# Kernel tuning notes

Measured on AMD Instinct MI355X. Metric: run time of the kernel, lower is better.

## Reference

```python
import jax, jax.numpy as jnp
import numpy as np

L_LAYERS = 2
EPS = 1e-6  # flax LayerNorm default epsilon


def _binop_reset(qi, qj):
    # S5 resettable associative scan element: (A, Bu, reset_flag)
    Ai, bi, ci = qi
    Aj, bj, cj = qj
    A = (Aj * Ai) * (1 - cj) + Aj * cj
    b = (Aj * bi + bj) * (1 - cj) + bj * cj
    c = ci * (1 - cj) + cj
    return A, b, c


def _layernorm(x, scale, bias):
    mu = jnp.mean(x, axis=-1, keepdims=True)
    var = jnp.var(x, axis=-1, keepdims=True)
    return (x - mu) * jax.lax.rsqrt(var + EPS) * scale + bias


def _s5_layer(x, resets, h0, lam_re, lam_im, B2, C2, Dv, log_step, nsc, nbi, gw, gb):
    # x: (B,T,H) float32; resets: (B,T) float32; h0: (B,1,P) complex64
    Bsz, T, H = x.shape
    P = lam_re.shape[0]
    skip = x
    xn = _layernorm(x, nsc, nbi)
    # ZOH discretization
    Lam = lam_re + 1j * lam_im                       # (P,)
    step = jnp.exp(log_step[:, 0])                   # (P,)
    Lam_bar = jnp.exp(Lam * step)                    # (P,)
    B_t = B2[..., 0] + 1j * B2[..., 1]               # (P,H)
    B_bar = ((Lam_bar - 1.0) / Lam)[:, None] * B_t   # (P,H)
    C_t = C2[..., 0] + 1j * C2[..., 1]               # (H,P)
    Bu = jnp.einsum('ph,bth->btp', B_bar, xn.astype(B_bar.dtype))  # (B,T,P) complex
    # prepend carry / identity elements, run reset-aware parallel scan over time
    ones = jnp.ones((Bsz, 1, P), dtype=Lam_bar.dtype)
    A_el = jnp.concatenate([ones, jnp.broadcast_to(Lam_bar, (Bsz, T, P))], axis=1)
    b_el = jnp.concatenate([h0, Bu], axis=1)
    c_el = jnp.concatenate([jnp.zeros((Bsz, 1, 1), x.dtype), resets[..., None]], axis=1)
    _, xs, _ = jax.lax.associative_scan(_binop_reset, (A_el, b_el, c_el), axis=1)
    xs = xs[:, 1:]                                   # (B,T,P) states
    h_new = xs[:, -1:, :]                            # (B,1,P) new carry
    ys = 2.0 * jnp.einsum('hp,btp->bth', C_t, xs).real  # conj_sym output
    y = ys + Dv * xn                                 # skip-through D
    # half_glu1 activation
    y = jax.nn.gelu(y)
    y = y * jax.nn.sigmoid(y @ gw + gb)
    return h_new, skip + y


def setup_inputs() -> dict:
    key = jax.random.key(0)
    B, T, OBS, H, P, L = 128, 1024, 512, 64, 128, L_LAYERS
    ks = jax.random.split(key, 10)
    obs = jax.random.normal(ks[0], (B, T, OBS), jnp.float32)
    dones = (jax.random.uniform(ks[1], (B, T)) < 0.02).astype(jnp.int32)
    hidden = jnp.zeros((L, B, 1, P, 2), jnp.float32)
    dense_w = jax.random.normal(ks[2], (OBS, H), jnp.float32) * np.float32(1.0 / np.sqrt(OBS))
    dense_b = jnp.zeros((H,), jnp.float32)
    Lambda_re = -(0.5 + jax.random.uniform(ks[3], (L, P), jnp.float32))  # stable (negative) real parts
    Lambda_im = np.float32(np.pi) * jax.random.normal(ks[4], (L, P), jnp.float32)
    Bp = jax.random.normal(ks[5], (L, P, H, 2), jnp.float32) * np.float32(1.0 / np.sqrt(H))
    Cp = jax.random.normal(ks[6], (L, H, P, 2), jnp.float32) * np.float32(1.0 / np.sqrt(P))
    D = jax.random.normal(ks[7], (L, H), jnp.float32)
    log_step = jax.random.uniform(ks[8], (L, P, 1), jnp.float32,
                                  minval=np.float32(np.log(0.001)), maxval=np.float32(np.log(0.1)))
    norm_scale = jnp.ones((L, H), jnp.float32)
    norm_bias = jnp.zeros((L, H), jnp.float32)
    glu_w = jax.random.normal(ks[9], (L, H, H), jnp.float32) * np.float32(1.0 / np.sqrt(H))
    glu_b = jnp.zeros((L, H), jnp.float32)
    return {"obs": obs, "dones": dones, "hidden": hidden, "dense_w": dense_w, "dense_b": dense_b,
            "Lambda_re": Lambda_re, "Lambda_im": Lambda_im, "Bp": Bp, "Cp": Cp, "D": D,
            "log_step": log_step, "norm_scale": norm_scale, "norm_bias": norm_bias,
            "glu_w": glu_w, "glu_b": glu_b}


def reference(obs, dones, hidden, dense_w, dense_b, Lambda_re, Lambda_im, Bp, Cp, D,
              log_step, norm_scale, norm_bias, glu_w, glu_b):
    x = obs @ dense_w + dense_b                      # dense_0 embedding (B,T,H)
    resets = dones.astype(x.dtype)
    h = hidden[..., 0] + 1j * hidden[..., 1]         # (L,B,1,P) complex carries
    new_h = []
    for l in range(L_LAYERS):
        hl, x = _s5_layer(x, resets, h[l], Lambda_re[l], Lambda_im[l], Bp[l], Cp[l], D[l],
                          log_step[l], norm_scale[l], norm_bias[l], glu_w[l], glu_b[l])
        new_h.append(hl)
    h_out = jnp.stack(new_h, axis=0)                 # (L,B,1,P) complex
    h_out = jnp.stack([h_out.real, h_out.imag], axis=-1)
    return h_out, x
```

## Files before the change

kernel.cpp:

```cpp
#include <hip/hip_runtime.h>

#define NB 128
#define NT 1024
#define NOBS 512
#define NH 64
#define NP 128
#define NM (NB*NT)
#define NN2 256
#define NCH 16
#define CHL 64

typedef short bf16x8 __attribute__((ext_vector_type(8)));
typedef float f32x4 __attribute__((ext_vector_type(4)));

#define CONST_OFF ((size_t)91226112)
#define CONST_STRIDE ((size_t)131072)
#define WTB_OFF   ((size_t)92274688)

__device__ __forceinline__ unsigned short f2b(float f) {
  unsigned int u = __float_as_uint(f);
  u = u + 0x7fffu + ((u >> 16) & 1u);
  return (unsigned short)(u >> 16);
}
__device__ __forceinline__ float b2f(unsigned short s) {
  return __uint_as_float(((unsigned int)s) << 16);
}

__global__ __launch_bounds__(256) void k_setup(const float* Lre, const float* Lim,
    const float* Bp, const float* Cp, const float* lstep, const float* gw,
    const float* dw, unsigned char* wsb) {
  int l = blockIdx.y;
  int idx = blockIdx.x * 256 + threadIdx.x;
  unsigned char* cb = wsb + CONST_OFF + (size_t)l * CONST_STRIDE;
  float2* lambar = (float2*)cb;
  unsigned short* Bglob = (unsigned short*)(cb + 1024);
  unsigned short* Cglob = (unsigned short*)(cb + 33792);
  unsigned short* gwT   = (unsigned short*)(cb + 66560);
  {
    int n = idx >> 6, h = idx & 63, p = n >> 1, c = n & 1;
    float step = expf(lstep[l * NP + p]);
    float re = Lre[l * NP + p], im = Lim[l * NP + p];
    float er = expf(re * step), ang = im * step;
    float lbr = er * cosf(ang), lbi = er * sinf(ang);
    if (h == 0 && c == 0) lambar[p] = make_float2(lbr, lbi);
    float den = re * re + im * im;
    float nr = lbr - 1.f, ni = lbi;
    float dr = (nr * re + ni * im) / den;
    float di = (ni * re - nr * im) / den;
    size_t bb = ((size_t)(l * NP + p) * NH + h) * 2;
    float b0 = Bp[bb + 0], b1 = Bp[bb + 1];
    float vr = dr * b0 - di * b1;
    float vi = dr * b1 + di * b0;
    Bglob[n * 64 + h] = f2b(c ? vi : vr);
  }
  {
    int h = idx >> 8, n = idx & 255, p = n >> 1;
    size_t base = ((size_t)(l * NH + h) * NP + p) * 2;
    float val = (n & 1) ? (-2.f * Cp[base + 1]) : (2.f * Cp[base + 0]);
    Cglob[h * 256 + n] = f2b(val);
  }
  if (idx < 4096) {
    int n = idx >> 6, k = idx & 63;
    gwT[n * 64 + k] = f2b(gw[(size_t)(l * NH + k) * NH + n]);
  }
  {
    int idx2 = l * 16384 + idx;
    int h = idx2 >> 9, k = idx2 & 511;
    ((unsigned short*)(wsb + WTB_OFF))[h * 512 + k] = f2b(dw[(size_t)k * NH + h]);
  }
}

__global__ __launch_bounds__(256) void k_dense(const float* __restrict__ obs,
    const unsigned short* __restrict__ wTb, const float* __restrict__ bias,
    float* __restrict__ xout) {
  __shared__ __align__(16) unsigned short As[128][72];
  __shared__ __align__(16) unsigned short Bs[64][72];
  int tid = threadIdx.x, lane = tid & 63, wv = tid >> 6;
  int row0 = blockIdx.x * 128;
  f32x4 acc[2][4] = {};
  float bcol[4];
#pragma unroll
  for (int ct = 0; ct < 4; ++ct) bcol[ct] = bias[ct * 16 + (lane & 15)];
  float4 ra[8];
  uint4 rb[2];
#pragma unroll
  for (int i = 0; i < 8; ++i) {
    int id = tid + i * 256;
    ra[i] = *(const float4*)(obs + (size_t)(row0 + (id >> 4)) * NOBS + (id & 15) * 4);
  }
#pragma unroll
  for (int i = 0; i < 2; ++i) {
    int id = tid + i * 256;
    rb[i] = *(const uint4*)(wTb + (id >> 3) * 512 + (id & 7) * 8);
  }
  for (int kt = 0; kt < 8; ++kt) {
#pragma unroll
    for (int i = 0; i < 8; ++i) {
      int id = tid + i * 256;
      ushort4 o; o.x = f2b(ra[i].x); o.y = f2b(ra[i].y); o.z = f2b(ra[i].z); o.w = f2b(ra[i].w);
      *(ushort4*)&As[id >> 4][(id & 15) * 4] = o;
    }
#pragma unroll
    for (int i = 0; i < 2; ++i) {
      int id = tid + i * 256;
      *(uint4*)&Bs[id >> 3][(id & 7) * 8] = rb[i];
    }
    __syncthreads();
    if (kt < 7) {
      int k0 = (kt + 1) * 64;
#pragma unroll
      for (int i = 0; i < 8; ++i) {
        int id = tid + i * 256;
        ra[i] = *(const float4*)(obs + (size_t)(row0 + (id >> 4)) * NOBS + k0 + (id & 15) * 4);
      }
#pragma unroll
      for (int i = 0; i < 2; ++i) {
        int id = tid + i * 256;
        rb[i] = *(const uint4*)(wTb + (id >> 3) * 512 + k0 + (id & 7) * 8);
      }
    }
#pragma unroll
    for (int kc = 0; kc < 2; ++kc) {
      bf16x8 a0 = *(const bf16x8*)&As[wv * 32 + (lane & 15)][kc * 32 + (lane >> 4) * 8];
      bf16x8 a1 = *(const bf16x8*)&As[wv * 32 + 16 + (lane & 15)][kc * 32 + (lane >> 4) * 8];
#pragma unroll
      for (int ct = 0; ct < 4; ++ct) {
        bf16x8 bb = *(const bf16x8*)&Bs[ct * 16 + (lane & 15)][kc * 32 + (lane >> 4) * 8];
        acc[0][ct] = __builtin_amdgcn_mfma_f32_16x16x32_bf16(a0, bb, acc[0][ct], 0, 0, 0);
        acc[1][ct] = __builtin_amdgcn_mfma_f32_16x16x32_bf16(a1, bb, acc[1][ct], 0, 0, 0);
      }
    }
    __syncthreads();
  }
  float* Os = (float*)&As[0][0];
#pragma unroll
  for (int pass = 0; pass < 2; ++pass) {
    if ((wv >> 1) == pass) {
#pragma unroll
      for (int rt = 0; rt < 2; ++rt)
#pragma unroll
        for (int ct = 0; ct < 4; ++ct)
#pragma unroll
          for (int e = 0; e < 4; ++e) {
            int rl = (wv & 1) * 32 + rt * 16 + (lane >> 4) * 4 + e;
            int col = ct * 16 + (lane & 15);
            Os[rl * 68 + col] = acc[rt][ct][e] + bcol[ct];
          }
    }
    __syncthreads();
    {
      int r = tid >> 2, seg = tid & 3;
#pragma unroll
      for (int i = 0; i < 4; ++i)
        *(float4*)(xout + (size_t)(row0 + pass * 64 + r) * NH + seg * 16 + i * 4) =
            *(const float4*)&Os[r * 68 + seg * 16 + i * 4];
    }
    __syncthreads();
  }
}

__global__ __launch_bounds__(512, 2) void k_2layers(float* __restrict__ x,
    const int* __restrict__ dones, const unsigned char* __restrict__ cb0,
    const float* __restrict__ hidden, float* __restrict__ hout,
    const float* __restrict__ nsc0, const float* __restrict__ nbi0,
    const float* __restrict__ Dv0, const float* __restrict__ gb0) {
  __shared__ __align__(16) unsigned short Bs[256][72];
  __shared__ __align__(16) unsigned short Cs[64][264];
  __shared__ __align__(16) unsigned short BuS[2][64][264];
  __shared__ __align__(16) unsigned short xnS[64][72];
  __shared__ __align__(16) unsigned short Ys[64][72];
  __shared__ int dS[1024];
  __shared__ float murs[4][64][2];
  int tid = threadIdx.x, lane = tid & 63, wv = tid >> 6;
  int b = blockIdx.x;

  dS[tid] = dones[b * NT + tid];
  dS[tid + 512] = dones[b * NT + 512 + tid];

#pragma unroll 1
  for (int l = 0; l < 2; ++l) {
    const unsigned char* cb = cb0 + (size_t)l * CONST_STRIDE;
    const float* nsc = nsc0 + l * NH;
    const float* nbi = nbi0 + l * NH;
    const float* Dv  = Dv0 + l * NH;
    const float* gb  = gb0 + l * NH;
    const unsigned short* Bglob = (const unsigned short*)(cb + 1024);
    const unsigned short* Cglob = (const unsigned short*)(cb + 33792);
    const unsigned short* gwT = (const unsigned short*)(cb + 66560);

    {
      int r = tid >> 1, h0 = (tid & 1) * 32;
#pragma unroll
      for (int i = 0; i < 4; ++i)
        *(uint4*)&Bs[r][h0 + i * 8] = *(const uint4*)(Bglob + r * 64 + h0 + i * 8);
    }
    {
      int r = tid >> 3, s0 = (tid & 7) * 32;
#pragma unroll
      for (int i = 0; i < 4; ++i)
        *(uint4*)&Cs[r][s0 + i * 8] = *(const uint4*)(Cglob + r * 256 + s0 + i * 8);
    }

    float4 pre0, pre1, pre2, pre3;
    float nscr[16], nbir[16];
    float lamr = 0.f, lami = 0.f, hr = 0.f, hi = 0.f;
    float Dr[4], nscc[4], nbic[4], gbr[4];
    if (tid < 256) {
      int q = tid & 3;
#pragma unroll
      for (int j = 0; j < 16; ++j) { nscr[j] = nsc[q * 16 + j]; nbir[j] = nbi[q * 16 + j]; }
      int r = tid >> 2;
      const float* xr = x + ((size_t)b * NT + r) * NH + q * 16;
      pre0 = *(const float4*)(xr);     pre1 = *(const float4*)(xr + 4);
      pre2 = *(const float4*)(xr + 8); pre3 = *(const float4*)(xr + 12);
    } else {
#pragma unroll
      for (int ct = 0; ct < 4; ++ct) {
        int col = ct * 16 + (lane & 15);
        Dr[ct] = Dv[col]; nscc[ct] = nsc[col]; nbic[ct] = nbi[col]; gbr[ct] = gb[col];
      }
      if (tid < 384) {
        int p = tid - 256;
        float2 lm = ((const float2*)cb)[p];
        lamr = lm.x; lami = lm.y;
        size_t hoff = (((size_t)l * NB + b) * NP + p) * 2;
        hr = hidden[hoff]; hi = hidden[hoff + 1];
      }
    }
    __syncthreads();

#pragma unroll 1
    for (int i = 0; i < NCH + 2; ++i) {
      float yreg[4][4], xres[4][4];
      if (tid < 256) {
        if (i < NCH) {
          float vv[16];
          *(float4*)&vv[0] = pre0;  *(float4*)&vv[4] = pre1;
          *(float4*)&vv[8] = pre2;  *(float4*)&vv[12] = pre3;
          int r = tid >> 2, q = tid & 3;
          if (i < NCH - 1) {
            const float* xr = x + ((size_t)b * NT + (i + 1) * CHL + r) * NH + q * 16;
            pre0 = *(const float4*)(xr);     pre1 = *(const float4*)(xr + 4);
            pre2 = *(const float4*)(xr + 8); pre3 = *(const float4*)(xr + 12);
          }
          float s = 0.f, s2 = 0.f;
#pragma unroll
          for (int j = 0; j < 16; ++j) { s += vv[j]; s2 += vv[j] * vv[j]; }
          s += __shfl_xor(s, 1); s2 += __shfl_xor(s2, 1);
          s += __shfl_xor(s, 2); s2 += __shfl_xor(s2, 2);
          float mu = s * 0.015625f;
          float var = s2 * 0.015625f - mu * mu;
          float rs = rsqrtf(var + 1e-6f);
          if (q == 0) { murs[i & 3][r][0] = mu; murs[i & 3][r][1] = rs; }
#pragma unroll
          for (int j = 0; j < 16; ++j)
            xnS[r][q * 16 + j] = f2b((vv[j] - mu) * rs * nscr[j] + nbir[j]);
        }
      } else if (i >= 2) {
        int j = i - 2, wv2 = wv - 4;
#pragma unroll
        for (int ct = 0; ct < 4; ++ct)
#pragma unroll
          for (int e = 0; e < 4; ++e) {
            int rl = wv2 * 16 + (lane >> 4) * 4 + e;
            xres[ct][e] = x[((size_t)b * NT + j * CHL + rl) * NH + ct * 16 + (lane & 15)];
          }
        f32x4 acc[4] = {};
        const unsigned short (*Bu)[264] = BuS[j & 1];
#pragma unroll
        for (int kc = 0; kc < 8; ++kc) {
          bf16x8 a = *(const bf16x8*)&Bu[wv2 * 16 + (lane & 15)][kc * 32 + (lane >> 4) * 8];
#pragma unroll
          for (int ct = 0; ct < 4; ++ct) {
            bf16x8 bbf = *(const bf16x8*)&Cs[ct * 16 + (lane & 15)][kc * 32 + (lane >> 4) * 8];
            acc[ct] = __builtin_amdgcn_mfma_f32_16x16x32_bf16(a, bbf, acc[ct], 0, 0, 0);
          }
        }
#pragma unroll
        for (int ct = 0; ct < 4; ++ct)
#pragma unroll
          for (int e = 0; e < 4; ++e) {
            int rl = wv2 * 16 + (lane >> 4) * 4 + e;
            float mu = murs[j & 3][rl][0], rs = murs[j & 3][rl][1];
            float xnv = (xres[ct][e] - mu) * rs * nscc[ct] + nbic[ct];
            float yv = acc[ct][e] + Dr[ct] * xnv;
            float t3 = 0.7978845608f * (yv + 0.044715f * yv * yv * yv);
            float u = __expf(2.f * t3);
            yv = 0.5f * yv * (2.f - 2.f / (u + 1.f));
            yreg[ct][e] = yv;
            Ys[rl][ct * 16 + (lane & 15)] = f2b(yv);
          }
      }
      __syncthreads();
      if (tid >= 256 && i >= 2) {
        int j = i - 2, wv2 = wv - 4;
        f32x4 gacc[4] = {};
#pragma unroll
        for (int kc = 0; kc < 2; ++kc) {
          bf16x8 a = *(const bf16x8*)&Ys[wv2 * 16 + (lane & 15)][kc * 32 + (lane >> 4) * 8];
#pragma unroll
          for (int ct = 0; ct < 4; ++ct) {
            bf16x8 bbf = *(const bf16x8*)(gwT + (ct * 16 + (lane & 15)) * 64 + kc * 32 + (lane >> 4) * 8);
            gacc[ct] = __builtin_amdgcn_mfma_f32_16x16x32_bf16(a, bbf, gacc[ct], 0, 0, 0);
          }
        }
#pragma unroll
        for (int ct = 0; ct < 4; ++ct)
#pragma unroll
          for (int e = 0; e < 4; ++e) {
            int rl = wv2 * 16 + (lane >> 4) * 4 + e;
            float g = gacc[ct][e] + gbr[ct];
            float sg = 1.f / (1.f + __expf(-g));
            x[((size_t)b * NT + j * CHL + rl) * NH + ct * 16 + (lane & 15)] =
                xres[ct][e] + yreg[ct][e] * sg;
          }
      }
      __syncthreads();
      if (tid < 256) {
        if (i < NCH) {
          f32x4 acc[16] = {};
#pragma unroll
          for (int kc = 0; kc < 2; ++kc) {
            bf16x8 a = *(const bf16x8*)&xnS[wv * 16 + (lane & 15)][kc * 32 + (lane >> 4) * 8];
#pragma unroll
            for (int ct = 0; ct < 16; ++ct) {
              bf16x8 bbf = *(const bf16x8*)&Bs[ct * 16 + (lane & 15)][kc * 32 + (lane >> 4) * 8];
              acc[ct] = __builtin_amdgcn_mfma_f32_16x16x32_bf16(a, bbf, acc[ct], 0, 0, 0);
            }
          }
          unsigned short (*Bu)[264] = BuS[i & 1];
#pragma unroll
          for (int ct = 0; ct < 16; ++ct)
#pragma unroll
            for (int e = 0; e < 4; ++e)
              Bu[wv * 16 + (lane >> 4) * 4 + e][ct * 16 + (lane & 15)] = f2b(acc[ct][e]);
        }
      } else if (tid < 384 && i >= 1 && i <= NCH) {
        int ch = i - 1, p = tid - 256;
        unsigned short (*Bu)[264] = BuS[ch & 1];
#pragma unroll 4
        for (int t = 0; t < CHL; ++t) {
          unsigned int u = *(const unsigned int*)&Bu[t][2 * p];
          float bur = b2f((unsigned short)(u & 0xffffu));
          float bui = b2f((unsigned short)(u >> 16));
          if (dS[ch * CHL + t]) { hr = bur; hi = bui; }
          else {
            float nr = lamr * hr - lami * hi + bur;
            hi = lamr * hi + lami * hr + bui; hr = nr;
          }
          *(unsigned int*)&Bu[t][2 * p] = (unsigned int)f2b(hr) | ((unsigned int)f2b(hi) << 16);
        }
        if (i == NCH) {
          size_t hoff = (((size_t)l * NB + b) * NP + p) * 2;
          hout[hoff] = hr; hout[hoff + 1] = hi;
        }
      }
      __syncthreads();
    }
  }
}

extern "C" void kernel_launch(void* const* d_in, const int* in_sizes, int n_in,
                              void* d_out, int out_size, void* d_ws, size_t ws_size,
                              hipStream_t stream) {
  const float* obs    = (const float*)d_in[0];
  const int*   dones  = (const int*)d_in[1];
  const float* hidden = (const float*)d_in[2];
  const float* dw     = (const float*)d_in[3];
  const float* db     = (const float*)d_in[4];
  const float* Lre    = (const float*)d_in[5];
  const float* Lim    = (const float*)d_in[6];
  const float* Bp     = (const float*)d_in[7];
  const float* Cp     = (const float*)d_in[8];
  const float* Dv     = (const float*)d_in[9];
  const float* lstep  = (const float*)d_in[10];
  const float* nsc    = (const float*)d_in[11];
  const float* nbi    = (const float*)d_in[12];
  const float* gw     = (const float*)d_in[13];
  const float* gb     = (const float*)d_in[14];

  float* hout = (float*)d_out;
  float* x = hout + (size_t)2 * NB * NP * 2;

  unsigned char* wsb = (unsigned char*)d_ws;
  unsigned short* wTb = (unsigned short*)(wsb + WTB_OFF);

  k_setup<<<dim3(64, 2), 256, 0, stream>>>(Lre, Lim, Bp, Cp, lstep, gw, dw, wsb);
  k_dense<<<NM / 128, 256, 0, stream>>>(obs, wTb, db, x);
  k_2layers<<<NB, 512, 0, stream>>>(x, dones, wsb + CONST_OFF, hidden, hout,
                                    nsc, nbi, Dv, gb);
}
```

Before: 320.8 us.

## Run the two S5 layers as concurrent blocks linked by per-chunk flags

```diff
diff --git a/kernel.cpp b/kernel.cpp
--- a/kernel.cpp
+++ b/kernel.cpp
@@ -1,4 +1,5 @@
 #include <hip/hip_runtime.h>
+#include <hip/hip_bf16.h>
 
 #define NB 128
 #define NT 1024
@@ -13,6 +14,7 @@
 typedef short bf16x8 __attribute__((ext_vector_type(8)));
 typedef float f32x4 __attribute__((ext_vector_type(4)));
 
+#define FLAG_OFF  ((size_t)83886080)
 #define CONST_OFF ((size_t)91226112)
 #define CONST_STRIDE ((size_t)131072)
 #define WTB_OFF   ((size_t)92274688)
@@ -24,6 +26,9 @@
 }
 __device__ __forceinline__ float b2f(unsigned short s) {
   return __uint_as_float(((unsigned int)s) << 16);
+}
+__device__ __forceinline__ unsigned int pk2(float lo, float hi) {
+  return (unsigned int)f2b(lo) | ((unsigned int)f2b(hi) << 16);
 }
 
 __global__ __launch_bounds__(256) void k_setup(const float* Lre, const float* Lim,
@@ -36,6 +41,7 @@
   unsigned short* Bglob = (unsigned short*)(cb + 1024);
   unsigned short* Cglob = (unsigned short*)(cb + 33792);
   unsigned short* gwT   = (unsigned short*)(cb + 66560);
+  if (l == 0 && idx < NB * NCH) ((int*)(wsb + FLAG_OFF))[idx] = 0;
   {
     int n = idx >> 6, h = idx & 63, p = n >> 1, c = n & 1;
     float step = expf(lstep[l * NP + p]);
@@ -159,11 +165,12 @@
   }
 }
 
-__global__ __launch_bounds__(512, 2) void k_2layers(float* __restrict__ x,
+__global__ __launch_bounds__(512, 1) void k_layer(float* __restrict__ x,
     const int* __restrict__ dones, const unsigned char* __restrict__ cb0,
     const float* __restrict__ hidden, float* __restrict__ hout,
     const float* __restrict__ nsc0, const float* __restrict__ nbi0,
-    const float* __restrict__ Dv0, const float* __restrict__ gb0) {
+    const float* __restrict__ Dv0, const float* __restrict__ gb0,
+    int* __restrict__ flagv) {
   __shared__ __align__(16) unsigned short Bs[256][72];
   __shared__ __align__(16) unsigned short Cs[64][264];
   __shared__ __align__(16) unsigned short BuS[2][64][264];
@@ -173,190 +180,204 @@
   __shared__ float murs[4][64][2];
   int tid = threadIdx.x, lane = tid & 63, wv = tid >> 6;
   int b = blockIdx.x;
-
+  int l = blockIdx.y;
+  const unsigned char* cb = cb0 + (size_t)l * CONST_STRIDE;
+  const float* nsc = nsc0 + l * NH;
+  const float* nbi = nbi0 + l * NH;
+  const float* Dv  = Dv0 + l * NH;
+  const float* gb  = gb0 + l * NH;
+  const unsigned short* Bglob = (const unsigned short*)(cb + 1024);
+  const unsigned short* Cglob = (const unsigned short*)(cb + 33792);
+  const unsigned short* gwT = (const unsigned short*)(cb + 66560);
+  int* flg = flagv + b * NCH;
+
+  {
+    int r = tid >> 1, h0 = (tid & 1) * 32;
+#pragma unroll
+    for (int i = 0; i < 4; ++i)
+      *(uint4*)&Bs[r][h0 + i * 8] = *(const uint4*)(Bglob + r * 64 + h0 + i * 8);
+  }
+  {
+    int r = tid >> 3, s0 = (tid & 7) * 32;
+#pragma unroll
+    for (int i = 0; i < 4; ++i)
+      *(uint4*)&Cs[r][s0 + i * 8] = *(const uint4*)(Cglob + r * 256 + s0 + i * 8);
+  }
   dS[tid] = dones[b * NT + tid];
   dS[tid + 512] = dones[b * NT + 512 + tid];
 
+  if (l == 1) {
+    while (__hip_atomic_load(&flg[0], __ATOMIC_RELAXED, __HIP_MEMORY_SCOPE_AGENT) == 0)
+      __builtin_amdgcn_s_sleep(8);
+    (void)__hip_atomic_load(&flg[0], __ATOMIC_ACQUIRE, __HIP_MEMORY_SCOPE_AGENT);
+  }
+
+  float4 pre0, pre1, pre2, pre3;
+  float nscr[16], nbir[16];
+  float lamr = 0.f, lami = 0.f, hr = 0.f, hi = 0.f;
+  float Dr[4], nscc[4], nbic[4], gbr[4];
+  if (tid < 256) {
+    int q = tid & 3;
+#pragma unroll
+    for (int j = 0; j < 16; ++j) { nscr[j] = nsc[q * 16 + j]; nbir[j] = nbi[q * 16 + j]; }
+    int r = tid >> 2;
+    const float* xr = x + ((size_t)b * NT + r) * NH + q * 16;
+    pre0 = *(const float4*)(xr);     pre1 = *(const float4*)(xr + 4);
+    pre2 = *(const float4*)(xr + 8); pre3 = *(const float4*)(xr + 12);
+  } else {
+#pragma unroll
+    for (int ct = 0; ct < 4; ++ct) {
+      int col = ct * 16 + (lane & 15);
+      Dr[ct] = Dv[col]; nscc[ct] = nsc[col]; nbic[ct] = nbi[col]; gbr[ct] = gb[col];
+    }
+    if (tid < 384) {
+      int p = tid - 256;
+      float2 lm = ((const float2*)cb)[p];
+      lamr = lm.x; lami = lm.y;
+      size_t hoff = (((size_t)l * NB + b) * NP + p) * 2;
+      hr = hidden[hoff]; hi = hidden[hoff + 1];
+    }
+  }
+  __syncthreads();
+
 #pragma unroll 1
-  for (int l = 0; l < 2; ++l) {
-    const unsigned char* cb = cb0 + (size_t)l * CONST_STRIDE;
-    const float* nsc = nsc0 + l * NH;
-    const float* nbi = nbi0 + l * NH;
-    const float* Dv  = Dv0 + l * NH;
-    const float* gb  = gb0 + l * NH;
-    const unsigned short* Bglob = (const unsigned short*)(cb + 1024);
-    const unsigned short* Cglob = (const unsigned short*)(cb + 33792);
-    const unsigned short* gwT = (const unsigned short*)(cb + 66560);
-
-    {
-      int r = tid >> 1, h0 = (tid & 1) * 32;
-#pragma unroll
-      for (int i = 0; i < 4; ++i)
-        *(uint4*)&Bs[r][h0 + i * 8] = *(const uint4*)(Bglob + r * 64 + h0 + i * 8);
-    }
-    {
-      int r = tid >> 3, s0 = (tid & 7) * 32;
-#pragma unroll
-      for (int i = 0; i < 4; ++i)
-        *(uint4*)&Cs[r][s0 + i * 8] = *(const uint4*)(Cglob + r * 256 + s0 + i * 8);
-    }
-
-    float4 pre0, pre1, pre2, pre3;
-    float nscr[16], nbir[16];
-    float lamr = 0.f, lami = 0.f, hr = 0.f, hi = 0.f;
-    float Dr[4], nscc[4], nbic[4], gbr[4];
+  for (int i = 0; i < NCH + 2; ++i) {
+    if (l == 1 && i < NCH - 1) {
+      while (__hip_atomic_load(&flg[i + 1], __ATOMIC_RELAXED, __HIP_MEMORY_SCOPE_AGENT) == 0)
+        __builtin_amdgcn_s_sleep(8);
+      (void)__hip_atomic_load(&flg[i + 1], __ATOMIC_ACQUIRE, __HIP_MEMORY_SCOPE_AGENT);
+    }
+    float yreg[4][4], xres[4][4];
     if (tid < 256) {
-      int q = tid & 3;
-#pragma unroll
-      for (int j = 0; j < 16; ++j) { nscr[j] = nsc[q * 16 + j]; nbir[j] = nbi[q * 16 + j]; }
-      int r = tid >> 2;
-      const float* xr = x + ((size_t)b * NT + r) * NH + q * 16;
-      pre0 = *(const float4*)(xr);     pre1 = *(const float4*)(xr + 4);
-      pre2 = *(const float4*)(xr + 8); pre3 = *(const float4*)(xr + 12);
-    } else {
-#pragma unroll
-      for (int ct = 0; ct < 4; ++ct) {
-        int col = ct * 16 + (lane & 15);
-        Dr[ct] = Dv[col]; nscc[ct] = nsc[col]; nbic[ct] = nbi[col]; gbr[ct] = gb[col];
-      }
-      if (tid < 384) {
-        int p = tid - 256;
-        float2 lm = ((const float2*)cb)[p];
-        lamr = lm.x; lami = lm.y;
+      if (i < NCH) {
+        float vv[16];
+        *(float4*)&vv[0] = pre0;  *(float4*)&vv[4] = pre1;
+        *(float4*)&vv[8] = pre2;  *(float4*)&vv[12] = pre3;
+        int r = tid >> 2, q = tid & 3;
+        if (i < NCH - 1) {
+          const float* xr = x + ((size_t)b * NT + (i + 1) * CHL + r) * NH + q * 16;
+          pre0 = *(const float4*)(xr);     pre1 = *(const float4*)(xr + 4);
+          pre2 = *(const float4*)(xr + 8); pre3 = *(const float4*)(xr + 12);
+        }
+        float s = 0.f, s2 = 0.f;
+#pragma unroll
+        for (int j = 0; j < 16; ++j) { s += vv[j]; s2 += vv[j] * vv[j]; }
+        s += __shfl_xor(s, 1); s2 += __shfl_xor(s2, 1);
+        s += __shfl_xor(s, 2); s2 += __shfl_xor(s2, 2);
+        float mu = s * 0.015625f;
+        float var = s2 * 0.015625f - mu * mu;
+        float rs = rsqrtf(var + 1e-6f);
+        if (q == 0) { murs[i & 3][r][0] = mu; murs[i & 3][r][1] = rs; }
+#pragma unroll
+        for (int k = 0; k < 8; ++k) {
+          float a0 = (vv[2 * k] - mu) * rs * nscr[2 * k] + nbir[2 * k];
+          float a1 = (vv[2 * k + 1] - mu) * rs * nscr[2 * k + 1] + nbir[2 * k + 1];
+          *(unsigned int*)&xnS[r][q * 16 + 2 * k] = pk2(a0, a1);
+        }
+      }
+    } else if (i >= 2) {
+      int j = i - 2, wv2 = wv - 4;
+#pragma unroll
+      for (int ct = 0; ct < 4; ++ct)
+#pragma unroll
+        for (int e = 0; e < 4; ++e) {
+          int rl = wv2 * 16 + (lane >> 4) * 4 + e;
+          xres[ct][e] = x[((size_t)b * NT + j * CHL + rl) * NH + ct * 16 + (lane & 15)];
+        }
+      f32x4 acc[4] = {};
+      const unsigned short (*Bu)[264] = BuS[j & 1];
+#pragma unroll
+      for (int kc = 0; kc < 8; ++kc) {
+        bf16x8 a = *(const bf16x8*)&Bu[wv2 * 16 + (lane & 15)][kc * 32 + (lane >> 4) * 8];
+#pragma unroll
+        for (int ct = 0; ct < 4; ++ct) {
+          bf16x8 bbf = *(const bf16x8*)&Cs[ct * 16 + (lane & 15)][kc * 32 + (lane >> 4) * 8];
+          acc[ct] = __builtin_amdgcn_mfma_f32_16x16x32_bf16(a, bbf, acc[ct], 0, 0, 0);
+        }
+      }
+#pragma unroll
+      for (int ct = 0; ct < 4; ++ct)
+#pragma unroll
+        for (int e = 0; e < 4; ++e) {
+          int rl = wv2 * 16 + (lane >> 4) * 4 + e;
+          float mu = murs[j & 3][rl][0], rs = murs[j & 3][rl][1];
+          float xnv = (xres[ct][e] - mu) * rs * nscc[ct] + nbic[ct];
+          float yv = acc[ct][e] + Dr[ct] * xnv;
+          float t3 = 0.7978845608f * (yv + 0.044715f * yv * yv * yv);
+          float u = __expf(2.f * t3);
+          yv = 0.5f * yv * (2.f - 2.f / (u + 1.f));
+          yreg[ct][e] = yv;
+          Ys[rl][ct * 16 + (lane & 15)] = f2b(yv);
+        }
+    }
+    __syncthreads();
+    if (tid >= 256 && i >= 2) {
+      int j = i - 2, wv2 = wv - 4;
+      f32x4 gacc[4] = {};
+#pragma unroll
+      for (int kc = 0; kc < 2; ++kc) {
+        bf16x8 a = *(const bf16x8*)&Ys[wv2 * 16 + (lane & 15)][kc * 32 + (lane >> 4) * 8];
+#pragma unroll
+        for (int ct = 0; ct < 4; ++ct) {
+          bf16x8 bbf = *(const bf16x8*)(gwT + (ct * 16 + (lane & 15)) * 64 + kc * 32 + (lane >> 4) * 8);
+          gacc[ct] = __builtin_amdgcn_mfma_f32_16x16x32_bf16(a, bbf, gacc[ct], 0, 0, 0);
+        }
+      }
+#pragma unroll
+      for (int ct = 0; ct < 4; ++ct)
+#pragma unroll
+        for (int e = 0; e < 4; ++e) {
+          int rl = wv2 * 16 + (lane >> 4) * 4 + e;
+          float g = gacc[ct][e] + gbr[ct];
+          float sg = 1.f / (1.f + __expf(-g));
+          x[((size_t)b * NT + j * CHL + rl) * NH + ct * 16 + (lane & 15)] =
+              xres[ct][e] + yreg[ct][e] * sg;
+        }
+    }
+    __syncthreads();
+    if (l == 0 && i >= 2 && tid == 511)
+      __hip_atomic_store(&flg[i - 2], 1, __ATOMIC_RELEASE, __HIP_MEMORY_SCOPE_AGENT);
+    if (tid < 256) {
+      if (i < NCH) {
+        f32x4 acc[16] = {};
+#pragma unroll
+        for (int kc = 0; kc < 2; ++kc) {
+          bf16x8 a = *(const bf16x8*)&xnS[wv * 16 + (lane & 15)][kc * 32 + (lane >> 4) * 8];
+#pragma unroll
+          for (int ct = 0; ct < 16; ++ct) {
+            bf16x8 bbf = *(const bf16x8*)&Bs[ct * 16 + (lane & 15)][kc * 32 + (lane >> 4) * 8];
+            acc[ct] = __builtin_amdgcn_mfma_f32_16x16x32_bf16(bbf, a, acc[ct], 0, 0, 0);
+          }
+        }
+        unsigned short (*Bu)[264] = BuS[i & 1];
+        int t = wv * 16 + (lane & 15), cb4 = (lane >> 4) * 4;
+#pragma unroll
+        for (int ct = 0; ct < 16; ++ct) {
+          *(unsigned int*)&Bu[t][ct * 16 + cb4]     = pk2(acc[ct][0], acc[ct][1]);
+          *(unsigned int*)&Bu[t][ct * 16 + cb4 + 2] = pk2(acc[ct][2], acc[ct][3]);
+        }
+      }
+    } else if (tid < 384 && i >= 1 && i <= NCH) {
+      int ch = i - 1, p = tid - 256;
+      unsigned short (*Bu)[264] = BuS[ch & 1];
+#pragma unroll 4
+      for (int t = 0; t < CHL; ++t) {
+        unsigned int u = *(const unsigned int*)&Bu[t][2 * p];
+        float bur = b2f((unsigned short)(u & 0xffffu));
+        float bui = b2f((unsigned short)(u >> 16));
+        if (dS[ch * CHL + t]) { hr = bur; hi = bui; }
+        else {
+          float nr = lamr * hr - lami * hi + bur;
+          hi = lamr * hi + lami * hr + bui; hr = nr;
+        }
+        *(unsigned int*)&Bu[t][2 * p] = pk2(hr, hi);
+      }
+      if (i == NCH) {
         size_t hoff = (((size_t)l * NB + b) * NP + p) * 2;
-        hr = hidden[hoff]; hi = hidden[hoff + 1];
-      }
-    }
-    __syncthreads();
-
-#pragma unroll 1
-    for (int i = 0; i < NCH + 2; ++i) {
-      float yreg[4][4], xres[4][4];
-      if (tid < 256) {
-        if (i < NCH) {
-          float vv[16];
-          *(float4*)&vv[0] = pre0;  *(float4*)&vv[4] = pre1;
-          *(float4*)&vv[8] = pre2;  *(float4*)&vv[12] = pre3;
-          int r = tid >> 2, q = tid & 3;
-          if (i < NCH - 1) {
-            const float* xr = x + ((size_t)b * NT + (i + 1) * CHL + r) * NH + q * 16;
-            pre0 = *(const float4*)(xr);     pre1 = *(const float4*)(xr + 4);
-            pre2 = *(const float4*)(xr + 8); pre3 = *(const float4*)(xr + 12);
-          }
-          float s = 0.f, s2 = 0.f;
-#pragma unroll
-          for (int j = 0; j < 16; ++j) { s += vv[j]; s2 += vv[j] * vv[j]; }
-          s += __shfl_xor(s, 1); s2 += __shfl_xor(s2, 1);
-          s += __shfl_xor(s, 2); s2 += __shfl_xor(s2, 2);
-          float mu = s * 0.015625f;
-          float var = s2 * 0.015625f - mu * mu;
-          float rs = rsqrtf(var + 1e-6f);
-          if (q == 0) { murs[i & 3][r][0] = mu; murs[i & 3][r][1] = rs; }
-#pragma unroll
-          for (int j = 0; j < 16; ++j)
-            xnS[r][q * 16 + j] = f2b((vv[j] - mu) * rs * nscr[j] + nbir[j]);
-        }
-      } else if (i >= 2) {
-        int j = i - 2, wv2 = wv - 4;
-#pragma unroll
-        for (int ct = 0; ct < 4; ++ct)
-#pragma unroll
-          for (int e = 0; e < 4; ++e) {
-            int rl = wv2 * 16 + (lane >> 4) * 4 + e;
-            xres[ct][e] = x[((size_t)b * NT + j * CHL + rl) * NH + ct * 16 + (lane & 15)];
-          }
-        f32x4 acc[4] = {};
-        const unsigned short (*Bu)[264] = BuS[j & 1];
-#pragma unroll
-        for (int kc = 0; kc < 8; ++kc) {
-          bf16x8 a = *(const bf16x8*)&Bu[wv2 * 16 + (lane & 15)][kc * 32 + (lane >> 4) * 8];
-#pragma unroll
-          for (int ct = 0; ct < 4; ++ct) {
-            bf16x8 bbf = *(const bf16x8*)&Cs[ct * 16 + (lane & 15)][kc * 32 + (lane >> 4) * 8];
-            acc[ct] = __builtin_amdgcn_mfma_f32_16x16x32_bf16(a, bbf, acc[ct], 0, 0, 0);
-          }
-        }
-#pragma unroll
-        for (int ct = 0; ct < 4; ++ct)
-#pragma unroll
-          for (int e = 0; e < 4; ++e) {
-            int rl = wv2 * 16 + (lane >> 4) * 4 + e;
-            float mu = murs[j & 3][rl][0], rs = murs[j & 3][rl][1];
-            float xnv = (xres[ct][e] - mu) * rs * nscc[ct] + nbic[ct];
-            float yv = acc[ct][e] + Dr[ct] * xnv;
-            float t3 = 0.7978845608f * (yv + 0.044715f * yv * yv * yv);
-            float u = __expf(2.f * t3);
-            yv = 0.5f * yv * (2.f - 2.f / (u + 1.f));
-            yreg[ct][e] = yv;
-            Ys[rl][ct * 16 + (lane & 15)] = f2b(yv);
-          }
-      }
-      __syncthreads();
-      if (tid >= 256 && i >= 2) {
-        int j = i - 2, wv2 = wv - 4;
-        f32x4 gacc[4] = {};
-#pragma unroll
-        for (int kc = 0; kc < 2; ++kc) {
-          bf16x8 a = *(const bf16x8*)&Ys[wv2 * 16 + (lane & 15)][kc * 32 + (lane >> 4) * 8];
-#pragma unroll
-          for (int ct = 0; ct < 4; ++ct) {
-            bf16x8 bbf = *(const bf16x8*)(gwT + (ct * 16 + (lane & 15)) * 64 + kc * 32 + (lane >> 4) * 8);
-            gacc[ct] = __builtin_amdgcn_mfma_f32_16x16x32_bf16(a, bbf, gacc[ct], 0, 0, 0);
-          }
-        }
-#pragma unroll
-        for (int ct = 0; ct < 4; ++ct)
-#pragma unroll
-          for (int e = 0; e < 4; ++e) {
-            int rl = wv2 * 16 + (lane >> 4) * 4 + e;
-            float g = gacc[ct][e] + gbr[ct];
-            float sg = 1.f / (1.f + __expf(-g));
-            x[((size_t)b * NT + j * CHL + rl) * NH + ct * 16 + (lane & 15)] =
-                xres[ct][e] + yreg[ct][e] * sg;
-          }
-      }
-      __syncthreads();
-      if (tid < 256) {
-        if (i < NCH) {
-          f32x4 acc[16] = {};
-#pragma unroll
-          for (int kc = 0; kc < 2; ++kc) {
-            bf16x8 a = *(const bf16x8*)&xnS[wv * 16 + (lane & 15)][kc * 32 + (lane >> 4) * 8];
-#pragma unroll
-            for (int ct = 0; ct < 16; ++ct) {
-              bf16x8 bbf = *(const bf16x8*)&Bs[ct * 16 + (lane & 15)][kc * 32 + (lane >> 4) * 8];
-              acc[ct] = __builtin_amdgcn_mfma_f32_16x16x32_bf16(a, bbf, acc[ct], 0, 0, 0);
-            }
-          }
-          unsigned short (*Bu)[264] = BuS[i & 1];
-#pragma unroll
-          for (int ct = 0; ct < 16; ++ct)
-#pragma unroll
-            for (int e = 0; e < 4; ++e)
-              Bu[wv * 16 + (lane >> 4) * 4 + e][ct * 16 + (lane & 15)] = f2b(acc[ct][e]);
-        }
-      } else if (tid < 384 && i >= 1 && i <= NCH) {
-        int ch = i - 1, p = tid - 256;
-        unsigned short (*Bu)[264] = BuS[ch & 1];
-#pragma unroll 4
-        for (int t = 0; t < CHL; ++t) {
-          unsigned int u = *(const unsigned int*)&Bu[t][2 * p];
-          float bur = b2f((unsigned short)(u & 0xffffu));
-          float bui = b2f((unsigned short)(u >> 16));
-          if (dS[ch * CHL + t]) { hr = bur; hi = bui; }
-          else {
-            float nr = lamr * hr - lami * hi + bur;
-            hi = lamr * hi + lami * hr + bui; hr = nr;
-          }
-          *(unsigned int*)&Bu[t][2 * p] = (unsigned int)f2b(hr) | ((unsigned int)f2b(hi) << 16);
-        }
-        if (i == NCH) {
-          size_t hoff = (((size_t)l * NB + b) * NP + p) * 2;
-          hout[hoff] = hr; hout[hoff + 1] = hi;
-        }
-      }
-      __syncthreads();
-    }
+        hout[hoff] = hr; hout[hoff + 1] = hi;
+      }
+    }
+    __syncthreads();
   }
 }
 
@@ -384,9 +405,10 @@
 
   unsigned char* wsb = (unsigned char*)d_ws;
   unsigned short* wTb = (unsigned short*)(wsb + WTB_OFF);
+  int* flagv = (int*)(wsb + FLAG_OFF);
 
   k_setup<<<dim3(64, 2), 256, 0, stream>>>(Lre, Lim, Bp, Cp, lstep, gw, dw, wsb);
   k_dense<<<NM / 128, 256, 0, stream>>>(obs, wTb, db, x);
-  k_2layers<<<NB, 512, 0, stream>>>(x, dones, wsb + CONST_OFF, hidden, hout,
-                                    nsc, nbi, Dv, gb);
-}
+  k_layer<<<dim3(NB, 2), 512, 0, stream>>>(x, dones, wsb + CONST_OFF, hidden, hout,
+                                           nsc, nbi, Dv, gb, flagv);
+}
```

Result: slower. 332.4 us (+3.6%).

## Fully unroll chunk scan with bitmask resets, register-cache GLU weights, pack bf16 stores

Applied to the files above, without the earlier changes.

```diff
diff --git a/kernel.cpp b/kernel.cpp
--- a/kernel.cpp
+++ b/kernel.cpp
@@ -24,6 +24,9 @@
 }
 __device__ __forceinline__ float b2f(unsigned short s) {
   return __uint_as_float(((unsigned int)s) << 16);
+}
+__device__ __forceinline__ unsigned int pk2(float lo, float hi) {
+  return (unsigned int)f2b(lo) | ((unsigned int)f2b(hi) << 16);
 }
 
 __global__ __launch_bounds__(256) void k_setup(const float* Lre, const float* Lim,
@@ -159,7 +162,7 @@
   }
 }
 
-__global__ __launch_bounds__(512, 2) void k_2layers(float* __restrict__ x,
+__global__ __launch_bounds__(512, 1) void k_2layers(float* __restrict__ x,
     const int* __restrict__ dones, const unsigned char* __restrict__ cb0,
     const float* __restrict__ hidden, float* __restrict__ hout,
     const float* __restrict__ nsc0, const float* __restrict__ nbi0,
@@ -169,13 +172,21 @@
   __shared__ __align__(16) unsigned short BuS[2][64][264];
   __shared__ __align__(16) unsigned short xnS[64][72];
   __shared__ __align__(16) unsigned short Ys[64][72];
-  __shared__ int dS[1024];
   __shared__ float murs[4][64][2];
+  __shared__ unsigned int dmask[32];
   int tid = threadIdx.x, lane = tid & 63, wv = tid >> 6;
   int b = blockIdx.x;
 
-  dS[tid] = dones[b * NT + tid];
-  dS[tid + 512] = dones[b * NT + 512 + tid];
+  {
+    unsigned long long m0 = __ballot(dones[b * NT + tid] != 0);
+    unsigned long long m1 = __ballot(dones[b * NT + 512 + tid] != 0);
+    if (lane == 0) {
+      dmask[wv * 2]          = (unsigned int)m0;
+      dmask[wv * 2 + 1]      = (unsigned int)(m0 >> 32);
+      dmask[16 + wv * 2]     = (unsigned int)m1;
+      dmask[16 + wv * 2 + 1] = (unsigned int)(m1 >> 32);
+    }
+  }
 
 #pragma unroll 1
   for (int l = 0; l < 2; ++l) {
@@ -205,6 +216,7 @@
     float nscr[16], nbir[16];
     float lamr = 0.f, lami = 0.f, hr = 0.f, hi = 0.f;
     float Dr[4], nscc[4], nbic[4], gbr[4];
+    bf16x8 gfr[2][4];
     if (tid < 256) {
       int q = tid & 3;
 #pragma unroll
@@ -219,6 +231,11 @@
         int col = ct * 16 + (lane & 15);
         Dr[ct] = Dv[col]; nscc[ct] = nsc[col]; nbic[ct] = nbi[col]; gbr[ct] = gb[col];
       }
+#pragma unroll
+      for (int kc = 0; kc < 2; ++kc)
+#pragma unroll
+        for (int ct = 0; ct < 4; ++ct)
+          gfr[kc][ct] = *(const bf16x8*)(gwT + (ct * 16 + (lane & 15)) * 64 + kc * 32 + (lane >> 4) * 8);
       if (tid < 384) {
         int p = tid - 256;
         float2 lm = ((const float2*)cb)[p];
@@ -253,8 +270,11 @@
           float rs = rsqrtf(var + 1e-6f);
           if (q == 0) { murs[i & 3][r][0] = mu; murs[i & 3][r][1] = rs; }
 #pragma unroll
-          for (int j = 0; j < 16; ++j)
-            xnS[r][q * 16 + j] = f2b((vv[j] - mu) * rs * nscr[j] + nbir[j]);
+          for (int k = 0; k < 8; ++k) {
+            float a0 = (vv[2 * k] - mu) * rs * nscr[2 * k] + nbir[2 * k];
+            float a1 = (vv[2 * k + 1] - mu) * rs * nscr[2 * k + 1] + nbir[2 * k + 1];
+            *(unsigned int*)&xnS[r][q * 16 + 2 * k] = pk2(a0, a1);
+          }
         }
       } else if (i >= 2) {
         int j = i - 2, wv2 = wv - 4;
@@ -299,10 +319,8 @@
         for (int kc = 0; kc < 2; ++kc) {
           bf16x8 a = *(const bf16x8*)&Ys[wv2 * 16 + (lane & 15)][kc * 32 + (lane >> 4) * 8];
 #pragma unroll
-          for (int ct = 0; ct < 4; ++ct) {
-            bf16x8 bbf = *(const bf16x8*)(gwT + (ct * 16 + (lane & 15)) * 64 + kc * 32 + (lane >> 4) * 8);
-            gacc[ct] = __builtin_amdgcn_mfma_f32_16x16x32_bf16(a, bbf, gacc[ct], 0, 0, 0);
-          }
+          for (int ct = 0; ct < 4; ++ct)
+            gacc[ct] = __builtin_amdgcn_mfma_f32_16x16x32_bf16(a, gfr[kc][ct], gacc[ct], 0, 0, 0);
         }
 #pragma unroll
         for (int ct = 0; ct < 4; ++ct)
@@ -325,32 +343,38 @@
 #pragma unroll
             for (int ct = 0; ct < 16; ++ct) {
               bf16x8 bbf = *(const bf16x8*)&Bs[ct * 16 + (lane & 15)][kc * 32 + (lane >> 4) * 8];
-              acc[ct] = __builtin_amdgcn_mfma_f32_16x16x32_bf16(a, bbf, acc[ct], 0, 0, 0);
+              acc[ct] = __builtin_amdgcn_mfma_f32_16x16x32_bf16(bbf, a, acc[ct], 0, 0, 0);
             }
           }
           unsigned short (*Bu)[264] = BuS[i & 1];
-#pragma unroll
-          for (int ct = 0; ct < 16; ++ct)
-#pragma unroll
-            for (int e = 0; e < 4; ++e)
-              Bu[wv * 16 + (lane >> 4) * 4 + e][ct * 16 + (lane & 15)] = f2b(acc[ct][e]);
+          int t = wv * 16 + (lane & 15), cb4 = (lane >> 4) * 4;
+#pragma unroll
+          for (int ct = 0; ct < 16; ++ct) {
+            *(unsigned int*)&Bu[t][ct * 16 + cb4]     = pk2(acc[ct][0], acc[ct][1]);
+            *(unsigned int*)&Bu[t][ct * 16 + cb4 + 2] = pk2(acc[ct][2], acc[ct][3]);
+          }
         }
       } else if (tid < 384 && i >= 1 && i <= NCH) {
         int ch = i - 1, p = tid - 256;
         unsigned short (*Bu)[264] = BuS[ch & 1];
-#pragma unroll 4
-        for (int t = 0; t < CHL; ++t) {
-          unsigned int u = *(const unsigned int*)&Bu[t][2 * p];
-          float bur = b2f((unsigned short)(u & 0xffffu));
-          float bui = b2f((unsigned short)(u >> 16));
-          if (dS[ch * CHL + t]) { hr = bur; hi = bui; }
-          else {
-            float nr = lamr * hr - lami * hi + bur;
-            hi = lamr * hi + lami * hr + bui; hr = nr;
-          }
-          *(unsigned int*)&Bu[t][2 * p] = (unsigned int)f2b(hr) | ((unsigned int)f2b(hi) << 16);
-        }
-        if (i == NCH) {
+        unsigned int m0 = dmask[ch * 2], m1 = dmask[ch * 2 + 1];
+        unsigned int v[64];
+#pragma unroll
+        for (int t = 0; t < 64; ++t) v[t] = *(const unsigned int*)&Bu[t][2 * p];
+#pragma unroll
+        for (int t = 0; t < 64; ++t) {
+          float bur = b2f((unsigned short)(v[t] & 0xffffu));
+          float bui = b2f((unsigned short)(v[t] >> 16));
+          bool d = (((t < 32 ? m0 : m1) >> (t & 31)) & 1u) != 0;
+          float nr = lamr * hr - lami * hi + bur;
+          float ni = lamr * hi + lami * hr + bui;
+          hr = d ? bur : nr;
+          hi = d ? bui : ni;
+          v[t] = pk2(hr, hi);
+        }
+#pragma unroll
+        for (int t = 0; t < 64; ++t) *(unsigned int*)&Bu[t][2 * p] = v[t];
+        if (ch == NCH - 1) {
           size_t hoff = (((size_t)l * NB + b) * NP + p) * 2;
           hout[hoff] = hr; hout[hoff + 1] = hi;
         }
```

Result: slower. 329.1 us (+2.6%).
